# Performance work log

Measured on AMD Instinct MI355X. Metric: run time of the kernel, lower is better.

Reference implementation:

```python
import jax, jax.numpy as jnp
import numpy as np

B, T, D, V, CD, NF = 2, 2048, 1024, 32000, 1024, 4
EPS_NORM = 1e-12
EPS_LN = 1e-5


def _gelu(x):
    return jax.nn.gelu(x, approximate=False)


def _l2norm(x):
    n = jnp.linalg.norm(x, axis=-1, keepdims=True)
    return x / jnp.maximum(n, EPS_NORM)


def setup_inputs() -> dict:
    key = jax.random.key(0)
    ks = jax.random.split(key, 24)
    s = 0.02
    inp = {
        "tokens": jax.random.randint(ks[0], (B, T), 0, V),
        "c_states": jax.random.normal(ks[1], (8, CD), dtype=jnp.float32),
        "embed": jax.random.normal(ks[2], (V, D), dtype=jnp.float32) * s,
        "pos_embed": jax.random.normal(ks[3], (T, D), dtype=jnp.float32) * s,
        # c_to_topo: Linear(c_dim,64) -> GELU -> Linear(64,2) -> Softplus (dead code in fwd, kept for completeness)
        "topo_W1": jax.random.normal(ks[4], (CD, 64), dtype=jnp.float32) * s,
        "topo_b1": jnp.zeros((64,), jnp.float32),
        "topo_W2": jax.random.normal(ks[5], (64, 2), dtype=jnp.float32) * s,
        "topo_b2": jnp.zeros((2,), jnp.float32),
        # c_to_thresh: Linear(c_dim,32) -> GELU -> Linear(32,NF) -> Sigmoid
        "thr_W1": jax.random.normal(ks[6], (CD, 32), dtype=jnp.float32) * s,
        "thr_b1": jnp.zeros((32,), jnp.float32),
        "thr_W2": jax.random.normal(ks[7], (32, NF), dtype=jnp.float32) * s,
        "thr_b2": jnp.zeros((NF,), jnp.float32),
        # simplex layers: NF x (Linear(2D,D) -> GELU -> Linear(D,D))
        "simp_W1": jax.random.normal(ks[8], (NF, 2 * D, D), dtype=jnp.float32) * s,
        "simp_b1": jnp.zeros((NF, D), jnp.float32),
        "simp_W2": jax.random.normal(ks[9], (NF, D, D), dtype=jnp.float32) * s,
        "simp_b2": jnp.zeros((NF, D), jnp.float32),
        # topo_integrate: Linear(D+2, 2D) -> GELU -> Linear(2D, D)
        "int_W1": jax.random.normal(ks[10], (D + 2, 2 * D), dtype=jnp.float32) * s,
        "int_b1": jnp.zeros((2 * D,), jnp.float32),
        "int_W2": jax.random.normal(ks[11], (2 * D, D), dtype=jnp.float32) * s,
        "int_b2": jnp.zeros((D,), jnp.float32),
        "ln_g": jnp.ones((D,), jnp.float32),
        "ln_b": jnp.zeros((D,), jnp.float32),
        "head_W": jax.random.normal(ks[12], (D, V), dtype=jnp.float32) * s,
    }
    return inp


def _forward(tokens, c_states, embed, pos_embed,
             topo_W1, topo_b1, topo_W2, topo_b2,
             thr_W1, thr_b1, thr_W2, thr_b2,
             simp_W1, simp_b1, simp_W2, simp_b2,
             int_W1, int_b1, int_W2, int_b2,
             ln_g, ln_b, head_W):
    b, t = tokens.shape
    x = embed[tokens] + pos_embed[jnp.arange(t)][None]          # [B,T,D]
    c_pooled = c_states.mean(axis=0)                            # [CD]
    thresholds = jax.nn.sigmoid(_gelu(c_pooled @ thr_W1 + thr_b1) @ thr_W2 + thr_b2)  # [NF]

    for level in range(NF):
        thresh = thresholds[level]
        x0 = x[0]                                               # [T,D] (module only uses batch elem 0)
        xn = _l2norm(x0)
        sim = xn @ xn.T                                         # [T,T]
        adj = jax.nn.sigmoid(10.0 * (sim - thresh))
        agg = adj @ x0                                          # dense message aggregation
        combined = jnp.concatenate([x0, agg], axis=-1)          # [T,2D]
        update = _gelu(combined @ simp_W1[level] + simp_b1[level]) @ simp_W2[level] + simp_b2[level]
        x = x + update[None] * 0.2                              # broadcast update across batch

    # approximate Betti numbers on detached embeddings
    xd = jax.lax.stop_gradient(x[0])
    xn = _l2norm(xd)
    sim = xn @ xn.T
    adj = jax.nn.sigmoid(10.0 * (sim - 0.5))
    degree = adj.sum(axis=-1)
    beta0 = (degree < 0.5).astype(jnp.float32).sum()
    n_edges = adj.sum() / 2.0
    beta1 = jax.nn.relu(n_edges - jnp.float32(t) + beta0 + 1.0)
    betti = jnp.stack([beta0, beta1])                           # [2]
    betti_exp = jnp.broadcast_to(betti[None, None, :], (b, t, 2))

    x = jnp.concatenate([x, betti_exp], axis=-1)                # [B,T,D+2]
    x = _gelu(x @ int_W1 + int_b1) @ int_W2 + int_b2            # [B,T,D]
    mu = x.mean(axis=-1, keepdims=True)
    var = x.var(axis=-1, keepdims=True)
    x = (x - mu) / jnp.sqrt(var + EPS_LN) * ln_g + ln_b
    return x @ head_W                                           # [B,T,V]


def reference(tokens, c_states, embed, pos_embed,
              topo_W1, topo_b1, topo_W2, topo_b2,
              thr_W1, thr_b1, thr_W2, thr_b2,
              simp_W1, simp_b1, simp_W2, simp_b2,
              int_W1, int_b1, int_W2, int_b2,
              ln_g, ln_b, head_W):
    return _forward(tokens, c_states, embed, pos_embed,
                    topo_W1, topo_b1, topo_W2, topo_b2,
                    thr_W1, thr_b1, thr_W2, thr_b2,
                    simp_W1, simp_b1, simp_W2, simp_b2,
                    int_W1, int_b1, int_W2, int_b2,
                    ln_g, ln_b, head_W)
```

## Files before the change

### kernel.cpp

```cpp
#include <hip/hip_runtime.h>

typedef __bf16 bf16;
using bf16x8 = __attribute__((ext_vector_type(8))) __bf16;
using bf16x4 = __attribute__((ext_vector_type(4))) __bf16;
using f32x4  = __attribute__((ext_vector_type(4))) float;

#define DEV __device__ __forceinline__

DEV float gelu_f(float x){ return 0.5f*x*(1.0f+erff(x*0.7071067811865475f)); }
DEV float sigm_f(float x){ return 1.0f/(1.0f+expf(-x)); }

DEV void gload16(const bf16* g, bf16* l){
    __builtin_amdgcn_global_load_lds(
        (const __attribute__((address_space(1))) void*)g,
        (__attribute__((address_space(3))) void*)l, 16, 0, 0);
}

enum { EPI_ADJ=0, EPI_BF16=1, EPI_GELU_BIAS=2, EPI_XUPD=3, EPI_BIAS_F32=4, EPI_F32=5 };

template<int BM,int BN,int WM,int WN,int EPI>
__global__ __launch_bounds__(WM*WN*64, 2)
void gemm_p(const bf16* __restrict__ A, const bf16* __restrict__ B,
            int M, int N, int K, void* __restrict__ Cout, int ldc,
            const float* __restrict__ bias, const float* __restrict__ scal, int sidx,
            float* __restrict__ xu0, float* __restrict__ xu1)
{
    constexpr int THREADS = WM*WN*64;
    constexpr int MR = BM/WM/16, NR = BN/WN/16;
    constexpr int ATILE = BM*64, BTILE = BN*64;
    constexpr int RR = THREADS/8;
    constexpr int VM = (BM+BN)/RR;
    __shared__ bf16 sm[2*(ATILE+BTILE)];

    const int nbm = M/BM, nbn = N/BN;
    const int nwg = nbm*nbn;
    int wg = blockIdx.x;
    wg = (wg&7)*(nwg>>3) + (wg>>3);
    const int by = wg % nbm, bx = wg / nbm;
    const int tid = threadIdx.x, lane = tid&63, wid = tid>>6;
    const int wm = wid / WN, wn = wid % WN;
    const int fr = lane&15, fq = lane>>4;

    const bf16* Ab = A + (long)(by*BM + (tid>>3))*K + (((tid&7) ^ ((tid>>3)&7))<<3);
    const bf16* Bb = B + (long)(bx*BN + (tid>>3))*K + (((tid&7) ^ ((tid>>3)&7))<<3);

    auto STAGE = [&](int tt, int cb){
        bf16* d = sm + cb*(ATILE+BTILE) + wid*512;
        const long ko = (long)tt*64;
#pragma unroll
        for (int g=0; g<BM/RR; ++g)
            gload16(Ab + (long)g*RR*K + ko, d + g*RR*64);
#pragma unroll
        for (int g=0; g<BN/RR; ++g)
            gload16(Bb + (long)g*RR*K + ko, d + ATILE + g*RR*64);
    };

    f32x4 acc[MR][NR] = {};
    const int nt = K >> 6;

    STAGE(0,0);
    STAGE(1,1);

    for (int t=0; t<nt; ++t){
        const bf16* bufA = sm + (t&1)*(ATILE+BTILE);
        const bf16* bufB = bufA + ATILE;
        if (t+1<nt){
            if constexpr (VM==6)      asm volatile("s_waitcnt vmcnt(6)" ::: "memory");
            else if constexpr (VM==8) asm volatile("s_waitcnt vmcnt(8)" ::: "memory");
            else                      asm volatile("s_waitcnt vmcnt(0)" ::: "memory");
        } else {
            asm volatile("s_waitcnt vmcnt(0)" ::: "memory");
        }
        __builtin_amdgcn_s_barrier();
        __builtin_amdgcn_sched_barrier(0);
#pragma unroll
        for (int ks=0; ks<2; ++ks){
            bf16x8 af[MR], bv[NR];
            const int ch = (((ks*4+fq) ^ (fr&7))<<3);
#pragma unroll
            for (int j=0;j<MR;++j)
                af[j] = *(const bf16x8*)&bufA[(wm*(MR*16) + j*16 + fr)*64 + ch];
#pragma unroll
            for (int j=0;j<NR;++j)
                bv[j] = *(const bf16x8*)&bufB[(wn*(NR*16) + j*16 + fr)*64 + ch];
            __builtin_amdgcn_s_setprio(1);
#pragma unroll
            for (int mi=0;mi<MR;++mi)
#pragma unroll
            for (int ni=0;ni<NR;++ni)
                acc[mi][ni] = __builtin_amdgcn_mfma_f32_16x16x32_bf16(
                    af[mi], bv[ni], acc[mi][ni], 0,0,0);
            __builtin_amdgcn_s_setprio(0);
        }
        asm volatile("s_waitcnt lgkmcnt(0)" ::: "memory");
        __builtin_amdgcn_s_barrier();
        if (t+2<nt) STAGE(t+2, t&1);
    }

    float thr = 0.f;
    if constexpr (EPI==EPI_ADJ) thr = scal[sidx];

#pragma unroll
    for (int mi=0;mi<MR;++mi){
#pragma unroll
        for (int ni=0;ni<NR;++ni){
            const int col = bx*BN + wn*(NR*16) + ni*16 + fr;
#pragma unroll
            for (int r=0;r<4;++r){
                const int row = by*BM + wm*(MR*16) + mi*16 + fq*4 + r;
                const float v = acc[mi][ni][r];
                const long ci = (long)row*ldc + col;
                if constexpr (EPI==EPI_ADJ)       ((bf16*)Cout)[ci] = (bf16)sigm_f(10.f*(v - thr));
                else if constexpr (EPI==EPI_BF16) ((bf16*)Cout)[ci] = (bf16)v;
                else if constexpr (EPI==EPI_GELU_BIAS) ((bf16*)Cout)[ci] = (bf16)gelu_f(v + bias[col]);
                else if constexpr (EPI==EPI_BIAS_F32)  ((float*)Cout)[ci] = v + bias[col];
                else if constexpr (EPI==EPI_F32)       ((float*)Cout)[ci] = v;
                else if constexpr (EPI==EPI_XUPD){
                    const float u = 0.2f*(v + bias[col]);
                    xu0[ci] += u;  xu1[ci] += u;
                }
            }
        }
    }
}

template<int EPI>
__global__ __launch_bounds__(512, 2)
void gemm8(const bf16* __restrict__ A, const bf16* __restrict__ B,
           int M, int N, int K, void* __restrict__ Cout, int ldc,
           const float* __restrict__ bias)
{
    __shared__ bf16 sm[65536];
    const int nbm = M>>8, nbn = N>>8;
    const int nwg = nbm*nbn;
    int wg = blockIdx.x;
    wg = (wg&7)*(nwg>>3) + (wg>>3);
    const int by = wg % nbm, bx = wg / nbm;
    const int tid = threadIdx.x, lane = tid&63, wid = tid>>6;
    const int wm = wid>>2, wn = wid&3;
    const int fr = lane&15, fq = lane>>4;

    const int srow = tid>>2, sch = tid&3;
    const bf16* Ag = A + (long)(by*256 + srow)*K + sch*8;
    const bf16* Bg = B + (long)(bx*256 + srow)*K + sch*8;

    auto STAGE = [&](int tt, int kh){
        const int rg = ((tt&1)*2 + kh)*8192;
        bf16* dA = sm + rg + wid*512;
        bf16* dB = sm + 32768 + rg + wid*512;
        const long ko = (long)tt*64 + kh*32;
        gload16(Ag + ko,          dA);
        gload16(Ag + 128*K + ko,  dA + 4096);
        gload16(Bg + ko,          dB);
        gload16(Bg + 128*K + ko,  dB + 4096);
    };

    f32x4 acc[8][4] = {};
    const int nt = K >> 6;

    STAGE(0,0); STAGE(0,1); STAGE(1,0);

    for (int t=0; t<nt; ++t){
#pragma unroll
        for (int s=0; s<2; ++s){
            if (t+1<nt)      asm volatile("s_waitcnt vmcnt(8)" ::: "memory");
            else if (s==0)   asm volatile("s_waitcnt vmcnt(4)" ::: "memory");
            else             asm volatile("s_waitcnt vmcnt(0)" ::: "memory");
            __builtin_amdgcn_s_barrier();
            __builtin_amdgcn_sched_barrier(0);
            if (s==0){ if (t+1<nt) STAGE(t+1,1); }
            else     { if (t+2<nt) STAGE(t+2,0); }
            __builtin_amdgcn_sched_barrier(0);

            const bf16* rA = sm + ((t&1)*2 + s)*8192;
            const bf16* rB = rA + 32768;
            bf16x8 af[8], bv[4];
#pragma unroll
            for (int j=0;j<8;++j)
                af[j] = *(const bf16x8*)&rA[(wm*128 + j*16 + fr)*32 + fq*8];
#pragma unroll
            for (int j=0;j<4;++j)
                bv[j] = *(const bf16x8*)&rB[(wn*64 + j*16 + fr)*32 + fq*8];
            asm volatile("s_waitcnt lgkmcnt(0)" ::: "memory");
            __builtin_amdgcn_sched_barrier(0);
            __builtin_amdgcn_s_setprio(1);
#pragma unroll
            for (int mi=0;mi<8;++mi)
#pragma unroll
            for (int ni=0;ni<4;++ni)
                acc[mi][ni] = __builtin_amdgcn_mfma_f32_16x16x32_bf16(
                    af[mi], bv[ni], acc[mi][ni], 0,0,0);
            __builtin_amdgcn_s_setprio(0);
            __builtin_amdgcn_sched_barrier(0);
        }
    }

#pragma unroll
    for (int mi=0;mi<8;++mi){
#pragma unroll
        for (int ni=0;ni<4;++ni){
            const int col = bx*256 + wn*64 + ni*16 + fr;
#pragma unroll
            for (int r=0;r<4;++r){
                const int row = by*256 + wm*128 + mi*16 + fq*4 + r;
                const float v = acc[mi][ni][r];
                const long ci = (long)row*ldc + col;
                if constexpr (EPI==EPI_F32)            ((float*)Cout)[ci] = v;
                else if constexpr (EPI==EPI_BIAS_F32)  ((float*)Cout)[ci] = v + bias[col];
                else                                   ((bf16*)Cout)[ci] = (bf16)v;
            }
        }
    }
}

__global__ void prep_kernel(const float* __restrict__ cs,
                            const float* __restrict__ W1, const float* __restrict__ b1,
                            const float* __restrict__ W2, const float* __restrict__ b2,
                            float* __restrict__ thrs)
{
    __shared__ float cp[1024];
    __shared__ float part[8][32];
    __shared__ float h[32];
    const int tid = threadIdx.x;
    for (int j = tid; j < 1024; j += 256){
        float s = 0.f;
#pragma unroll
        for (int r = 0; r < 8; r++) s += cs[r*1024 + j];
        cp[j] = s * 0.125f;
    }
    __syncthreads();
    const int t = tid & 31, g = tid >> 5;
    float p = 0.f;
    for (int j = g*128; j < g*128+128; j++) p += cp[j] * W1[j*32 + t];
    part[g][t] = p;
    __syncthreads();
    if (tid < 32){
        float s = b1[tid];
#pragma unroll
        for (int q=0;q<8;q++) s += part[q][tid];
        h[tid] = gelu_f(s);
    }
    __syncthreads();
    if (tid < 4){
        float z = b2[tid];
        for (int k=0;k<32;k++) z += h[k]*W2[k*4 + tid];
        thrs[tid] = sigm_f(z);
    }
    if (tid == 4) thrs[4] = 0.5f;
}

__global__ void embed_kernel(const int* __restrict__ tok, const float* __restrict__ emb,
                             const float* __restrict__ pos, float* __restrict__ x)
{
    const long i = (long)blockIdx.x*256 + threadIdx.x;
    const int  d4 = i & 255;
    const long bt = i >> 8;
    const int  t  = (int)(bt & 2047);
    const int  token = tok[bt];
    f32x4 e = *(const f32x4*)(emb + (long)token*1024 + d4*4);
    f32x4 p = *(const f32x4*)(pos + (long)t*1024 + d4*4);
    *(f32x4*)(x + i*4) = e + p;
}

__global__ void transpose_f2b(const float* __restrict__ in, int ldin,
                              bf16* __restrict__ out, int ldout, int R, int C)
{
    __shared__ float tile[32][33];
    const int nbx = C >> 5;
    const int bx = blockIdx.x % nbx, by = blockIdx.x / nbx;
    const int tx = threadIdx.x & 31, ty = threadIdx.x >> 5;
#pragma unroll
    for (int i=0;i<32;i+=8)
        tile[ty+i][tx] = in[(long)(by*32+ty+i)*ldin + bx*32+tx];
    __syncthreads();
#pragma unroll
    for (int i=0;i<32;i+=8)
        out[(long)(bx*32+ty+i)*ldout + by*32+tx] = (bf16)tile[tx][ty+i];
}

__global__ void rownorm_kernel(const float* __restrict__ x, bf16* __restrict__ xn,
                               bf16* __restrict__ x0b, int ld0)
{
    const long t = blockIdx.x; const int tid = threadIdx.x;
    f32x4 v = *(const f32x4*)(x + t*1024 + tid*4);
    float s = v.x*v.x + v.y*v.y + v.z*v.z + v.w*v.w;
#pragma unroll
    for (int o=32;o>0;o>>=1) s += __shfl_down(s, o);
    __shared__ float red[4];
    if ((tid&63)==0) red[tid>>6] = s;
    __syncthreads();
    const float tot = red[0]+red[1]+red[2]+red[3];
    const float inv = 1.0f / fmaxf(sqrtf(tot), 1e-12f);
    bf16x4 a, b;
    a[0]=(bf16)(v.x*inv); a[1]=(bf16)(v.y*inv); a[2]=(bf16)(v.z*inv); a[3]=(bf16)(v.w*inv);
    b[0]=(bf16)v.x; b[1]=(bf16)v.y; b[2]=(bf16)v.z; b[3]=(bf16)v.w;
    *(bf16x4*)(xn  + t*1024 + tid*4) = a;
    *(bf16x4*)(x0b + t*ld0  + tid*4) = b;
}

__global__ void degree_kernel(const bf16* __restrict__ adj, float* __restrict__ deg)
{
    const long t = blockIdx.x; const int tid = threadIdx.x;
    bf16x8 v = *(const bf16x8*)(adj + t*2048 + tid*8);
    float s = 0.f;
#pragma unroll
    for (int j=0;j<8;j++) s += (float)v[j];
#pragma unroll
    for (int o=32;o>0;o>>=1) s += __shfl_down(s, o);
    __shared__ float red[4];
    if ((tid&63)==0) red[tid>>6] = s;
    __syncthreads();
    if (tid==0) deg[t] = red[0]+red[1]+red[2]+red[3];
}

__global__ void betti_kernel(const float* __restrict__ deg, float* __restrict__ betti)
{
    const int tid = threadIdx.x;
    float s = 0.f, c = 0.f;
#pragma unroll
    for (int i=0;i<8;i++){
        const float d = deg[tid*8 + i];
        s += d;  c += (d < 0.5f) ? 1.f : 0.f;
    }
#pragma unroll
    for (int o=32;o>0;o>>=1){ s += __shfl_down(s,o); c += __shfl_down(c,o); }
    __shared__ float ss[4], cc[4];
    if ((tid&63)==0){ ss[tid>>6]=s; cc[tid>>6]=c; }
    __syncthreads();
    if (tid==0){
        const float S = ss[0]+ss[1]+ss[2]+ss[3];
        const float C = cc[0]+cc[1]+cc[2]+cc[3];
        const float ne = 0.5f*S;
        const float b1 = ne - 2048.f + C + 1.f;
        betti[0] = C;
        betti[1] = b1 > 0.f ? b1 : 0.f;
    }
}

__global__ void b1eff_kernel(const float* __restrict__ ib1, const float* __restrict__ iW1,
                             const float* __restrict__ betti, float* __restrict__ out)
{
    const int j = blockIdx.x*256 + threadIdx.x;
    out[j] = ib1[j] + betti[0]*iW1[(long)1024*2048 + j] + betti[1]*iW1[(long)1025*2048 + j];
}

__global__ void f2b_kernel(const float* __restrict__ in, bf16* __restrict__ out)
{
    const long i = (long)blockIdx.x*256 + threadIdx.x;
    f32x4 a = *(const f32x4*)(in + i*8);
    f32x4 c = *(const f32x4*)(in + i*8 + 4);
    bf16x8 o;
    o[0]=(bf16)a.x; o[1]=(bf16)a.y; o[2]=(bf16)a.z; o[3]=(bf16)a.w;
    o[4]=(bf16)c.x; o[5]=(bf16)c.y; o[6]=(bf16)c.z; o[7]=(bf16)c.w;
    *(bf16x8*)(out + i*8) = o;
}

__global__ void ln_kernel(const float* __restrict__ y, const float* __restrict__ g,
                          const float* __restrict__ b, bf16* __restrict__ out)
{
    const long t = blockIdx.x; const int tid = threadIdx.x;
    f32x4 v = *(const f32x4*)(y + t*1024 + tid*4);
    float s  = v.x+v.y+v.z+v.w;
    float s2 = v.x*v.x+v.y*v.y+v.z*v.z+v.w*v.w;
#pragma unroll
    for (int o=32;o>0;o>>=1){ s += __shfl_down(s,o); s2 += __shfl_down(s2,o); }
    __shared__ float ss[4], qq[4];
    if ((tid&63)==0){ ss[tid>>6]=s; qq[tid>>6]=s2; }
    __syncthreads();
    const float S = ss[0]+ss[1]+ss[2]+ss[3], Q = qq[0]+qq[1]+qq[2]+qq[3];
    const float mu  = S * (1.f/1024.f);
    const float var = Q * (1.f/1024.f) - mu*mu;
    const float inv = rsqrtf(var + 1e-5f);
    f32x4 gv = *(const f32x4*)(g + tid*4);
    f32x4 bv = *(const f32x4*)(b + tid*4);
    bf16x4 o;
    o[0] = (bf16)((v.x - mu)*inv*gv.x + bv.x);
    o[1] = (bf16)((v.y - mu)*inv*gv.y + bv.y);
    o[2] = (bf16)((v.z - mu)*inv*gv.z + bv.z);
    o[3] = (bf16)((v.w - mu)*inv*gv.w + bv.w);
    *(bf16x4*)(out + t*1024 + tid*4) = o;
}

extern "C" void kernel_launch(void* const* d_in, const int* in_sizes, int n_in,
                              void* d_out, int out_size, void* d_ws, size_t ws_size,
                              hipStream_t stream)
{
    const int*   tokens = (const int*)  d_in[0];
    const float* cstate = (const float*)d_in[1];
    const float* embedW = (const float*)d_in[2];
    const float* posW   = (const float*)d_in[3];
    const float* thrW1  = (const float*)d_in[8];
    const float* thrb1  = (const float*)d_in[9];
    const float* thrW2  = (const float*)d_in[10];
    const float* thrb2  = (const float*)d_in[11];
    const float* simpW1 = (const float*)d_in[12];
    const float* simpb1 = (const float*)d_in[13];
    const float* simpW2 = (const float*)d_in[14];
    const float* simpb2 = (const float*)d_in[15];
    const float* intW1  = (const float*)d_in[16];
    const float* intb1  = (const float*)d_in[17];
    const float* intW2  = (const float*)d_in[18];
    const float* intb2  = (const float*)d_in[19];
    const float* lng    = (const float*)d_in[20];
    const float* lnb    = (const float*)d_in[21];
    const float* headW  = (const float*)d_in[22];
    float* out = (float*)d_out;

    size_t off = 0;
    auto carve = [&](size_t bytes) -> void* {
        void* p = (char*)d_ws + off;
        off += (bytes + 255) & ~(size_t)255;
        return p;
    };
    float* x_f32   = (float*)carve(16777216);
    bf16*  xn      = (bf16*) carve(4194304);
    bf16*  x0T     = (bf16*) carve(4194304);
    bf16*  comb    = (bf16*) carve(8388608);
    bf16*  adj     = (bf16*) carve(8388608);
    bf16*  h1      = (bf16*) carve(4194304);
    bf16*  xb      = (bf16*) carve(8388608);
    bf16*  w1T     = (bf16*) carve(16777216);
    bf16*  w2T     = (bf16*) carve(8388608);
    bf16*  i1T     = (bf16*) carve(4194304);
    bf16*  i2T     = (bf16*) carve(4194304);
    bf16*  hT      = (bf16*) carve(65536000);
    float* degree  = (float*)carve(8192);
    float* b1eff   = (float*)carve(8192);
    float* thrs    = (float*)carve(64);
    float* betti   = (float*)carve(64);
    bf16*  h2  = comb;
    float* yv  = x_f32;
    bf16*  xln = xn;

    const dim3 blk(256);
    const dim3 blk512(512);

    prep_kernel<<<1, blk, 0, stream>>>(cstate, thrW1, thrb1, thrW2, thrb2, thrs);
    embed_kernel<<<4096, blk, 0, stream>>>(tokens, embedW, posW, x_f32);

    for (int l=0;l<4;l++)
        transpose_f2b<<<(1024/32)*(2048/32), blk, 0, stream>>>(
            simpW1 + (long)l*2048*1024, 1024, w1T + (long)l*1024*2048, 2048, 2048, 1024);
    for (int l=0;l<4;l++)
        transpose_f2b<<<(1024/32)*(1024/32), blk, 0, stream>>>(
            simpW2 + (long)l*1024*1024, 1024, w2T + (long)l*1024*1024, 1024, 1024, 1024);
    transpose_f2b<<<(2048/32)*(1024/32), blk, 0, stream>>>(intW1, 2048, i1T, 1024, 1024, 2048);
    transpose_f2b<<<(1024/32)*(2048/32), blk, 0, stream>>>(intW2, 1024, i2T, 2048, 2048, 1024);
    transpose_f2b<<<(32000/32)*(1024/32), blk, 0, stream>>>(headW, 32000, hT, 1024, 1024, 32000);

    for (int l=0;l<4;l++){
        rownorm_kernel<<<2048, blk, 0, stream>>>(x_f32, xn, comb, 2048);
        transpose_f2b<<<(1024/32)*(2048/32), blk, 0, stream>>>(x_f32, 1024, x0T, 2048, 2048, 1024);
        gemm_p<128,128,2,2,EPI_ADJ><<<16*16, blk, 0, stream>>>(
            xn, xn, 2048, 2048, 1024, adj, 2048, nullptr, thrs, l, nullptr, nullptr);
        gemm_p<64,128,2,2,EPI_BF16><<<32*8, blk, 0, stream>>>(
            adj, x0T, 2048, 1024, 2048, comb + 1024, 2048, nullptr, nullptr, 0, nullptr, nullptr);
        gemm_p<64,128,2,2,EPI_GELU_BIAS><<<32*8, blk, 0, stream>>>(
            comb, w1T + (long)l*1024*2048, 2048, 1024, 2048, h1, 1024,
            simpb1 + l*1024, nullptr, 0, nullptr, nullptr);
        gemm_p<64,128,2,2,EPI_XUPD><<<32*8, blk, 0, stream>>>(
            h1, w2T + (long)l*1024*1024, 2048, 1024, 1024, nullptr, 1024,
            simpb2 + l*1024, nullptr, 0, x_f32, x_f32 + (long)2048*1024);
    }

    rownorm_kernel<<<2048, blk, 0, stream>>>(x_f32, xn, comb, 2048);
    gemm_p<128,128,2,2,EPI_ADJ><<<16*16, blk, 0, stream>>>(
        xn, xn, 2048, 2048, 1024, adj, 2048, nullptr, thrs, 4, nullptr, nullptr);
    degree_kernel<<<2048, blk, 0, stream>>>(adj, degree);
    betti_kernel<<<1, blk, 0, stream>>>(degree, betti);
    b1eff_kernel<<<8, blk, 0, stream>>>(intb1, intW1, betti, b1eff);

    f2b_kernel<<<2048, blk, 0, stream>>>(x_f32, xb);
    gemm_p<128,128,2,2,EPI_GELU_BIAS><<<32*16, blk, 0, stream>>>(
        xb, i1T, 4096, 2048, 1024, h2, 2048, b1eff, nullptr, 0, nullptr, nullptr);
    gemm_p<128,128,2,2,EPI_BIAS_F32><<<32*8, blk, 0, stream>>>(
        h2, i2T, 4096, 1024, 2048, yv, 1024, intb2, nullptr, 0, nullptr, nullptr);
    ln_kernel<<<4096, blk, 0, stream>>>(yv, lng, lnb, xln);
    gemm8<EPI_F32><<<16*125, blk512, 0, stream>>>(
        xln, hT, 4096, 32000, 1024, out, 32000, nullptr);
}
```

Measured before the change: 916.1 us.

## Restructure 256x256 GEMM main loop into quadrant-staged pipeline with XOR-swizzled LDS

Result: faster. 880.4 us (-3.9%).

```diff
diff --git a/kernel.cpp b/kernel.cpp
--- a/kernel.cpp
+++ b/kernel.cpp
@@ -6,6 +6,7 @@
 using f32x4  = __attribute__((ext_vector_type(4))) float;
 
 #define DEV __device__ __forceinline__
+#define SCHED_FENCE() __builtin_amdgcn_sched_barrier(0)
 
 DEV float gelu_f(float x){ return 0.5f*x*(1.0f+erff(x*0.7071067811865475f)); }
 DEV float sigm_f(float x){ return 1.0f/(1.0f+expf(-x)); }
@@ -140,59 +141,98 @@
     const int wm = wid>>2, wn = wid&3;
     const int fr = lane&15, fq = lane>>4;
 
-    const int srow = tid>>2, sch = tid&3;
-    const bf16* Ag = A + (long)(by*256 + srow)*K + sch*8;
-    const bf16* Bg = B + (long)(bx*256 + srow)*K + sch*8;
-
-    auto STAGE = [&](int tt, int kh){
-        const int rg = ((tt&1)*2 + kh)*8192;
-        bf16* dA = sm + rg + wid*512;
-        bf16* dB = sm + 32768 + rg + wid*512;
-        const long ko = (long)tt*64 + kh*32;
-        gload16(Ag + ko,          dA);
-        gload16(Ag + 128*K + ko,  dA + 4096);
-        gload16(Bg + ko,          dB);
-        gload16(Bg + 128*K + ko,  dB + 4096);
+    const bf16* Ag = A + (long)(by*256 + (tid>>3))*K + (((tid&7) ^ ((tid>>3)&7))<<3);
+    const bf16* Bg = B + (long)(bx*256 + (tid>>3))*K + (((tid&7) ^ ((tid>>3)&7))<<3);
+
+    auto SA = [&](int tt, int h){
+        bf16* d = sm + (tt&1)*32768 + wid*512;
+        const long ko = (long)tt*64;
+        gload16(Ag + (long)(h*64)*K + ko,       d + h*4096);
+        gload16(Ag + (long)(128+h*64)*K + ko,   d + 8192 + h*4096);
     };
+    auto SB = [&](int tt, int h){
+        bf16* d = sm + (tt&1)*32768 + 16384 + wid*512;
+        const long ko = (long)tt*64;
+#pragma unroll
+        for (int g=0; g<2; ++g)
+            gload16(Bg + (long)(h*2+g)*64*K + ko, d + (h*2+g)*4096);
+    };
 
     f32x4 acc[8][4] = {};
+    bf16x8 aCur[8], b0[4], b1[4];
     const int nt = K >> 6;
 
-    STAGE(0,0); STAGE(0,1); STAGE(1,0);
+    SA(0,0); SB(0,0); SA(0,1); SB(0,1);
+    SA(1,0); SB(1,0); SA(1,1);
+    SCHED_FENCE();
 
     for (int t=0; t<nt; ++t){
-#pragma unroll
-        for (int s=0; s<2; ++s){
-            if (t+1<nt)      asm volatile("s_waitcnt vmcnt(8)" ::: "memory");
-            else if (s==0)   asm volatile("s_waitcnt vmcnt(4)" ::: "memory");
-            else             asm volatile("s_waitcnt vmcnt(0)" ::: "memory");
-            __builtin_amdgcn_s_barrier();
-            __builtin_amdgcn_sched_barrier(0);
-            if (s==0){ if (t+1<nt) STAGE(t+1,1); }
-            else     { if (t+2<nt) STAGE(t+2,0); }
-            __builtin_amdgcn_sched_barrier(0);
-
-            const bf16* rA = sm + ((t&1)*2 + s)*8192;
-            const bf16* rB = rA + 32768;
-            bf16x8 af[8], bv[4];
-#pragma unroll
-            for (int j=0;j<8;++j)
-                af[j] = *(const bf16x8*)&rA[(wm*128 + j*16 + fr)*32 + fq*8];
+        const bf16* bufA = sm + (t&1)*32768;
+        const bf16* bufB = bufA + 16384;
+
+        auto LDA = [&](int mh){
+#pragma unroll
+            for (int ks=0;ks<2;++ks){
+                const int ch = (((ks*4+fq) ^ (fr&7))<<3);
+#pragma unroll
+                for (int j=0;j<4;++j)
+                    aCur[ks*4+j] = *(const bf16x8*)&bufA[(wm*128 + mh*64 + j*16 + fr)*64 + ch];
+            }
+        };
+        auto LDB = [&](int nh, bf16x8* dst){
+#pragma unroll
+            for (int ks=0;ks<2;++ks){
+                const int ch = (((ks*4+fq) ^ (fr&7))<<3);
+#pragma unroll
+                for (int j=0;j<2;++j)
+                    dst[ks*2+j] = *(const bf16x8*)&bufB[(wn*64 + nh*32 + j*16 + fr)*64 + ch];
+            }
+        };
+        auto QMFMA = [&](int mh, int nh, bf16x8* bArr){
+            __builtin_amdgcn_s_setprio(1);
+#pragma unroll
+            for (int ks=0;ks<2;++ks)
 #pragma unroll
             for (int j=0;j<4;++j)
-                bv[j] = *(const bf16x8*)&rB[(wn*64 + j*16 + fr)*32 + fq*8];
-            asm volatile("s_waitcnt lgkmcnt(0)" ::: "memory");
-            __builtin_amdgcn_sched_barrier(0);
-            __builtin_amdgcn_s_setprio(1);
-#pragma unroll
-            for (int mi=0;mi<8;++mi)
-#pragma unroll
-            for (int ni=0;ni<4;++ni)
-                acc[mi][ni] = __builtin_amdgcn_mfma_f32_16x16x32_bf16(
-                    af[mi], bv[ni], acc[mi][ni], 0,0,0);
+#pragma unroll
+            for (int jj=0;jj<2;++jj)
+                acc[mh*4+j][nh*2+jj] = __builtin_amdgcn_mfma_f32_16x16x32_bf16(
+                    aCur[ks*4+j], bArr[ks*2+jj], acc[mh*4+j][nh*2+jj], 0,0,0);
             __builtin_amdgcn_s_setprio(0);
-            __builtin_amdgcn_sched_barrier(0);
-        }
+            SCHED_FENCE();
+        };
+
+        if (t+1<nt) asm volatile("s_waitcnt vmcnt(6)" ::: "memory");
+        else        asm volatile("s_waitcnt vmcnt(0)" ::: "memory");
+        __builtin_amdgcn_s_barrier();
+        SCHED_FENCE();
+        if (t+1<nt) SB(t+1,1);
+        SCHED_FENCE();
+        LDA(0); LDB(0, b0);
+        asm volatile("s_waitcnt lgkmcnt(0)" ::: "memory");
+        SCHED_FENCE();
+        QMFMA(0,0,b0);
+        __builtin_amdgcn_s_barrier();
+        SCHED_FENCE();
+        if (t+2<nt) SA(t+2,0);
+        SCHED_FENCE();
+        LDB(1, b1);
+        asm volatile("s_waitcnt lgkmcnt(0)" ::: "memory");
+        SCHED_FENCE();
+        QMFMA(0,1,b1);
+        __builtin_amdgcn_s_barrier();
+        SCHED_FENCE();
+        if (t+2<nt) SB(t+2,0);
+        SCHED_FENCE();
+        LDA(1);
+        asm volatile("s_waitcnt lgkmcnt(0)" ::: "memory");
+        SCHED_FENCE();
+        QMFMA(1,1,b1);
+        __builtin_amdgcn_s_barrier();
+        SCHED_FENCE();
+        if (t+2<nt) SA(t+2,1);
+        SCHED_FENCE();
+        QMFMA(1,0,b0);
     }
 
 #pragma unroll
```
